# Kernel tuning notes

Measured on AMD Instinct MI355X. Metric: run time of the kernel, lower is better.

The kernel has to match this reference:

```python
import jax, jax.numpy as jnp
from jax import lax
import numpy as np

B, CIN, H, W_IN = 16, 1, 224, 224
COUT = 18 * 16  # 18 parallel convs, 16 channels each, fused
K = 3
HOUT, WOUT = H - K + 1, W_IN - K + 1  # VALID padding


def setup_inputs() -> dict:
    key = jax.random.key(0)
    k1, k2, k3 = jax.random.split(key, 3)
    x1 = jax.random.normal(k1, (B, CIN, H, W_IN), dtype=jnp.float32)
    W = jax.random.normal(k2, (COUT, CIN, K, K), dtype=jnp.float32)
    bias = jax.random.normal(k3, (1, COUT, HOUT, WOUT), dtype=jnp.float32)
    return {"x1": x1, "W": W, "bias": bias}


def reference(x1, W, bias):
    # Fused equivalent of 18 separate 1->16 conv2d ops + channel concat:
    # a single 1->288 VALID conv, then full-tensor bias add + ReLU epilogue.
    y = lax.conv_general_dilated(
        x1, W,
        window_strides=(1, 1),
        padding="VALID",
        dimension_numbers=("NCHW", "OIHW", "NCHW"),
    )  # (B, 288, 222, 222)
    return jax.nn.relu(y + bias)
```

## Files before the change

### kernel.cpp

```cpp
#include <hip/hip_runtime.h>


constexpr int Bn    = 16;
constexpr int COUT  = 288;
constexpr int Hin   = 224;
constexpr int Win   = 224;
constexpr int HOUT  = 222;
constexpr int WOUT  = 222;
constexpr int PLANE = HOUT * WOUT;
constexpr int NF4   = PLANE / 4;
constexpr int XPLANE = Hin * Win;

__global__ __launch_bounds__(256) void conv_bias_relu(
    const float* __restrict__ x,
    const float* __restrict__ w,
    const float* __restrict__ bias,
    float* __restrict__ out)
{
    const int f4 = blockIdx.x * blockDim.x + threadIdx.x;
    if (f4 >= NF4) return;
    const int f   = f4 * 4;
    const int co0 = blockIdx.y * 4;

    float wv[4][9];
    #pragma unroll
    for (int c = 0; c < 4; ++c)
        #pragma unroll
        for (int k = 0; k < 9; ++k)
            wv[c][k] = w[(co0 + c) * 9 + k];

    int off[4];
    #pragma unroll
    for (int j = 0; j < 4; ++j) {
        unsigned fj = (unsigned)(f + j);
        unsigned ho = fj / 222u;
        unsigned wo = fj - ho * 222u;
        off[j] = (int)(ho * 224u + wo);
    }

    float4 bv[4];
    #pragma unroll
    for (int c = 0; c < 4; ++c)
        bv[c] = *reinterpret_cast<const float4*>(bias + (size_t)(co0 + c) * PLANE + f);

    for (int b = 0; b < Bn; ++b) {
        const float* xb = x + b * XPLANE;

        float acc[4][4];
        #pragma unroll
        for (int c = 0; c < 4; ++c) {
            acc[c][0] = bv[c].x; acc[c][1] = bv[c].y;
            acc[c][2] = bv[c].z; acc[c][3] = bv[c].w;
        }

        #pragma unroll
        for (int j = 0; j < 4; ++j) {
            float xv[9];
            const float* xp = xb + off[j];
            #pragma unroll
            for (int kh = 0; kh < 3; ++kh)
                #pragma unroll
                for (int kw = 0; kw < 3; ++kw)
                    xv[kh * 3 + kw] = xp[kh * 224 + kw];

            #pragma unroll
            for (int c = 0; c < 4; ++c)
                #pragma unroll
                for (int k = 0; k < 9; ++k)
                    acc[c][j] = fmaf(wv[c][k], xv[k], acc[c][j]);
        }

        #pragma unroll
        for (int c = 0; c < 4; ++c) {
            float4 o;
            o.x = fmaxf(acc[c][0], 0.f);
            o.y = fmaxf(acc[c][1], 0.f);
            o.z = fmaxf(acc[c][2], 0.f);
            o.w = fmaxf(acc[c][3], 0.f);
            *reinterpret_cast<float4*>(
                out + (size_t)(b * COUT + co0 + c) * PLANE + f) = o;
        }
    }
}

extern "C" void kernel_launch(void* const* d_in, const int* in_sizes, int n_in,
                              void* d_out, int out_size, void* d_ws, size_t ws_size,
                              hipStream_t stream) {
    const float* x    = (const float*)d_in[0];
    const float* w    = (const float*)d_in[1];
    const float* bias = (const float*)d_in[2];
    float* out        = (float*)d_out;

    dim3 block(256);
    dim3 grid((NF4 + 255) / 256, COUT / 4);
    conv_bias_relu<<<grid, block, 0, stream>>>(x, w, bias, out);
}
```

Measured before the change: 1.141 ms.

## Stage input rows in swizzled LDS with register prefetch across batches

Each block now loads the 8 input rows its output positions need into shared memory, using an XOR swizzle to reduce bank conflicts. The 36 per-thread global gathers become LDS reads through precomputed swizzled offsets. The next batch's rows are prefetched into registers while the current batch is computed. This adds two barriers per batch iteration and extra register pressure from the offset table.

```diff
diff --git a/kernel.cpp b/kernel.cpp
--- a/kernel.cpp
+++ b/kernel.cpp
@@ -11,16 +11,42 @@
 constexpr int NF4   = PLANE / 4;
 constexpr int XPLANE = Hin * Win;
 
+constexpr int POS_PER_BLOCK = 1024;
+constexpr int XROWS  = 8;
+constexpr int LDSW   = XROWS * Win;
+constexpr int NCHUNK = LDSW / 4;
+constexpr int CPR    = Win / 4;
+
+__device__ __forceinline__ float4 swz_permute(float4 v, int g) {
+    const bool s1 = (g & 1) != 0;
+    const bool s2 = (g & 2) != 0;
+    float ax = s1 ? v.y : v.x, ay = s1 ? v.x : v.y;
+    float az = s1 ? v.w : v.z, aw = s1 ? v.z : v.w;
+    float4 d;
+    d.x = s2 ? az : ax; d.y = s2 ? aw : ay;
+    d.z = s2 ? ax : az; d.w = s2 ? ay : aw;
+    return d;
+}
+
 __global__ __launch_bounds__(256) void conv_bias_relu(
     const float* __restrict__ x,
     const float* __restrict__ w,
     const float* __restrict__ bias,
     float* __restrict__ out)
 {
-    const int f4 = blockIdx.x * blockDim.x + threadIdx.x;
-    if (f4 >= NF4) return;
-    const int f   = f4 * 4;
+    __shared__ __align__(16) float lds[LDSW];
+
+    const int tid = threadIdx.x;
+    const int bx  = blockIdx.x;
     const int co0 = blockIdx.y * 4;
+
+    const int  f4r    = bx * 256 + tid;
+    const bool active = f4r < NF4;
+    const int  f4     = active ? f4r : (NF4 - 1);
+    const int  f      = f4 * 4;
+
+    const int f0  = bx * POS_PER_BLOCK;
+    const int ho0 = f0 / WOUT;
 
     float wv[4][9];
     #pragma unroll
@@ -29,22 +55,58 @@
         for (int k = 0; k < 9; ++k)
             wv[c][k] = w[(co0 + c) * 9 + k];
 
-    int off[4];
-    #pragma unroll
-    for (int j = 0; j < 4; ++j) {
-        unsigned fj = (unsigned)(f + j);
-        unsigned ho = fj / 222u;
-        unsigned wo = fj - ho * 222u;
-        off[j] = (int)(ho * 224u + wo);
-    }
-
     float4 bv[4];
     #pragma unroll
     for (int c = 0; c < 4; ++c)
         bv[c] = *reinterpret_cast<const float4*>(bias + (size_t)(co0 + c) * PLANE + f);
 
+    int ra[36];
+    #pragma unroll
+    for (int j = 0; j < 4; ++j) {
+        const int fj = f + j;
+        const int ho = fj / WOUT;
+        const int wo = fj - ho * WOUT;
+        const int base = (ho - ho0) * Win + wo;
+        #pragma unroll
+        for (int kh = 0; kh < 3; ++kh)
+            #pragma unroll
+            for (int kw = 0; kw < 3; ++kw) {
+                const int wd = base + kh * Win + kw;
+                ra[j * 9 + kh * 3 + kw] = wd ^ ((wd >> 5) & 3);
+            }
+    }
+
+    const int  ch0  = tid;
+    const int  ch1  = tid + 256;
+    const bool has2 = ch1 < NCHUNK;
+
+    const int r0    = ch0 / CPR;
+    const int c0w   = (ch0 - r0 * CPR) * 4;
+    const int srow0 = min(ho0 + r0, Hin - 1);
+    const int soff0 = srow0 * Win + c0w;
+    const int g0    = (ch0 >> 3) & 3;
+
+    const int r1    = ch1 / CPR;
+    const int c1w   = (ch1 - r1 * CPR) * 4;
+    const int srow1 = min(ho0 + r1, Hin - 1);
+    const int soff1 = srow1 * Win + c1w;
+    const int g1    = (ch1 >> 3) & 3;
+
+    float4 p0, p1;
+    p0 = *reinterpret_cast<const float4*>(x + soff0);
+    if (has2) p1 = *reinterpret_cast<const float4*>(x + soff1);
+
     for (int b = 0; b < Bn; ++b) {
-        const float* xb = x + b * XPLANE;
+        __syncthreads();
+        reinterpret_cast<float4*>(lds)[ch0] = swz_permute(p0, g0);
+        if (has2) reinterpret_cast<float4*>(lds)[ch1] = swz_permute(p1, g1);
+        __syncthreads();
+
+        if (b + 1 < Bn) {
+            const float* xb = x + (b + 1) * XPLANE;
+            p0 = *reinterpret_cast<const float4*>(xb + soff0);
+            if (has2) p1 = *reinterpret_cast<const float4*>(xb + soff1);
+        }
 
         float acc[4][4];
         #pragma unroll
@@ -56,13 +118,9 @@
         #pragma unroll
         for (int j = 0; j < 4; ++j) {
             float xv[9];
-            const float* xp = xb + off[j];
             #pragma unroll
-            for (int kh = 0; kh < 3; ++kh)
-                #pragma unroll
-                for (int kw = 0; kw < 3; ++kw)
-                    xv[kh * 3 + kw] = xp[kh * 224 + kw];
-
+            for (int k = 0; k < 9; ++k)
+                xv[k] = lds[ra[j * 9 + k]];
             #pragma unroll
             for (int c = 0; c < 4; ++c)
                 #pragma unroll
@@ -70,15 +128,17 @@
                     acc[c][j] = fmaf(wv[c][k], xv[k], acc[c][j]);
         }
 
-        #pragma unroll
-        for (int c = 0; c < 4; ++c) {
-            float4 o;
-            o.x = fmaxf(acc[c][0], 0.f);
-            o.y = fmaxf(acc[c][1], 0.f);
-            o.z = fmaxf(acc[c][2], 0.f);
-            o.w = fmaxf(acc[c][3], 0.f);
-            *reinterpret_cast<float4*>(
-                out + (size_t)(b * COUT + co0 + c) * PLANE + f) = o;
+        if (active) {
+            #pragma unroll
+            for (int c = 0; c < 4; ++c) {
+                float4 o;
+                o.x = fmaxf(acc[c][0], 0.f);
+                o.y = fmaxf(acc[c][1], 0.f);
+                o.z = fmaxf(acc[c][2], 0.f);
+                o.w = fmaxf(acc[c][3], 0.f);
+                *reinterpret_cast<float4*>(
+                    out + (size_t)(b * COUT + co0 + c) * PLANE + f) = o;
+            }
         }
     }
 }
```

Measured after the change: 961.6 us. 1.19x faster.

## Tile output as 4 vertical rows per thread with column-per-lane mapping

Applied to the files above, without the earlier changes.

Restructures the thread mapping so each lane owns one output column and computes four consecutive output rows, loading a 6x3 input window that is reused across the rows. This replaces the flat 4-consecutive-pixel mapping with its per-pixel division and 36 input loads. The cost is scalar (non-float4) stores and bias loads, plus idle lanes at the 222-column edge, since 222 is not a multiple of 64. The kernel is dominated by output writes (~908MB), so store coalescing matters most.

```diff
diff --git a/kernel.cpp b/kernel.cpp
--- a/kernel.cpp
+++ b/kernel.cpp
@@ -1,84 +1,98 @@
 #include <hip/hip_runtime.h>
 
 
-constexpr int Bn    = 16;
-constexpr int COUT  = 288;
-constexpr int Hin   = 224;
-constexpr int Win   = 224;
-constexpr int HOUT  = 222;
-constexpr int WOUT  = 222;
-constexpr int PLANE = HOUT * WOUT;
-constexpr int NF4   = PLANE / 4;
+constexpr int Bn     = 16;
+constexpr int COUT   = 288;
+constexpr int Hin    = 224;
+constexpr int Win    = 224;
+constexpr int HOUT   = 222;
+constexpr int WOUT   = 222;
+constexpr int PLANE  = HOUT * WOUT;
 constexpr int XPLANE = Hin * Win;
 
 __global__ __launch_bounds__(256) void conv_bias_relu(
     const float* __restrict__ x,
-    const float* __restrict__ w,
+    const float* __restrict__ wgt,
     const float* __restrict__ bias,
     float* __restrict__ out)
 {
-    const int f4 = blockIdx.x * blockDim.x + threadIdx.x;
-    if (f4 >= NF4) return;
-    const int f   = f4 * 4;
-    const int co0 = blockIdx.y * 4;
+    const int tid  = threadIdx.x;
+    const int lane = tid & 63;
+    const int wid  = tid >> 6;
 
-    float wv[4][9];
+    const int c0  = blockIdx.x * 64;
+    const int rb  = blockIdx.y * 16 + wid * 4;
+    const int co0 = blockIdx.z * 4;
+
+    const int  c     = c0 + lane;
+    const bool colok = (c < WOUT);
+    const int  ceff  = colok ? c : (WOUT - 1);
+
+    float wt[4][9];
     #pragma unroll
-    for (int c = 0; c < 4; ++c)
+    for (int q = 0; q < 4; ++q)
         #pragma unroll
         for (int k = 0; k < 9; ++k)
-            wv[c][k] = w[(co0 + c) * 9 + k];
+            wt[q][k] = wgt[(co0 + q) * 9 + k];
 
-    int off[4];
+    int rofx[6];
     #pragma unroll
-    for (int j = 0; j < 4; ++j) {
-        unsigned fj = (unsigned)(f + j);
-        unsigned ho = fj / 222u;
-        unsigned wo = fj - ho * 222u;
-        off[j] = (int)(ho * 224u + wo);
+    for (int k = 0; k < 6; ++k)
+        rofx[k] = min(rb + k, Hin - 1) * Win + ceff;
+
+    bool rowok[4];
+    int  rofo[4];
+    #pragma unroll
+    for (int p = 0; p < 4; ++p) {
+        rowok[p] = (rb + p) < HOUT;
+        rofo[p]  = min(rb + p, HOUT - 1) * WOUT;
     }
 
-    float4 bv[4];
+    float bv[4][4];
     #pragma unroll
-    for (int c = 0; c < 4; ++c)
-        bv[c] = *reinterpret_cast<const float4*>(bias + (size_t)(co0 + c) * PLANE + f);
+    for (int q = 0; q < 4; ++q)
+        #pragma unroll
+        for (int p = 0; p < 4; ++p)
+            bv[q][p] = bias[(size_t)(co0 + q) * PLANE + rofo[p] + ceff];
 
     for (int b = 0; b < Bn; ++b) {
         const float* xb = x + b * XPLANE;
 
+        float xr[6][3];
+        #pragma unroll
+        for (int k = 0; k < 6; ++k)
+            #pragma unroll
+            for (int j = 0; j < 3; ++j)
+                xr[k][j] = xb[rofx[k] + j];
+
         float acc[4][4];
         #pragma unroll
-        for (int c = 0; c < 4; ++c) {
-            acc[c][0] = bv[c].x; acc[c][1] = bv[c].y;
-            acc[c][2] = bv[c].z; acc[c][3] = bv[c].w;
-        }
+        for (int q = 0; q < 4; ++q)
+            #pragma unroll
+            for (int p = 0; p < 4; ++p)
+                acc[q][p] = bv[q][p];
 
         #pragma unroll
-        for (int j = 0; j < 4; ++j) {
-            float xv[9];
-            const float* xp = xb + off[j];
+        for (int p = 0; p < 4; ++p)
             #pragma unroll
             for (int kh = 0; kh < 3; ++kh)
                 #pragma unroll
-                for (int kw = 0; kw < 3; ++kw)
-                    xv[kh * 3 + kw] = xp[kh * 224 + kw];
+                for (int kw = 0; kw < 3; ++kw) {
+                    const float xv = xr[p + kh][kw];
+                    #pragma unroll
+                    for (int q = 0; q < 4; ++q)
+                        acc[q][p] = fmaf(wt[q][kh * 3 + kw], xv, acc[q][p]);
+                }
 
+        if (colok) {
             #pragma unroll
-            for (int c = 0; c < 4; ++c)
+            for (int q = 0; q < 4; ++q) {
+                float* ob = out + (size_t)(b * COUT + co0 + q) * PLANE + c;
                 #pragma unroll
-                for (int k = 0; k < 9; ++k)
-                    acc[c][j] = fmaf(wv[c][k], xv[k], acc[c][j]);
-        }
-
-        #pragma unroll
-        for (int c = 0; c < 4; ++c) {
-            float4 o;
-            o.x = fmaxf(acc[c][0], 0.f);
-            o.y = fmaxf(acc[c][1], 0.f);
-            o.z = fmaxf(acc[c][2], 0.f);
-            o.w = fmaxf(acc[c][3], 0.f);
-            *reinterpret_cast<float4*>(
-                out + (size_t)(b * COUT + co0 + c) * PLANE + f) = o;
+                for (int p = 0; p < 4; ++p)
+                    if (rowok[p])
+                        ob[(rb + p) * WOUT] = fmaxf(acc[q][p], 0.f);
+            }
         }
     }
 }
@@ -92,6 +106,8 @@
     float* out        = (float*)d_out;
 
     dim3 block(256);
-    dim3 grid((NF4 + 255) / 256, COUT / 4);
+    dim3 grid((WOUT + 63) / 64,
+              (HOUT + 15) / 16,
+              COUT / 4);
     conv_bias_relu<<<grid, block, 0, stream>>>(x, w, bias, out);
 }
```

Result: no change. 1.154 ms (+1.2%).
